# Performance work log

Measured on AMD Instinct MI355X. Metric: run time of the kernel, lower is better.

## Reference

```python
import jax, jax.numpy as jnp
import numpy as np

T, N, D, H = 128, 512, 1024, 1024
LN_EPS = 1e-5


def setup_inputs() -> dict:
    key = jax.random.key(0)
    ks = jax.random.split(key, 6)
    x = jax.random.normal(ks[0], (T * N, D), jnp.float32)
    hxs = jax.random.normal(ks[1], (N, 1, H), jnp.float32)
    # binary done-masks (float, mostly 1.0 = keep hidden state, 0.0 = episode reset)
    masks = (jax.random.uniform(ks[2], (T * N, 1)) < 0.95).astype(jnp.float32)
    s = 1.0 / np.sqrt(H)
    # PyTorch GRU packed gates, order (r, z, n): weight_ih_l0 [3H, D], weight_hh_l0 [3H, H]
    W_ih = jax.random.normal(ks[3], (3 * H, D), jnp.float32) * s
    W_hh = jax.random.normal(ks[4], (3 * H, H), jnp.float32) * s
    b_ih = jnp.zeros((3 * H,), jnp.float32)  # module inits biases to 0
    b_hh = jnp.zeros((3 * H,), jnp.float32)
    gamma = jnp.ones((H,), jnp.float32)
    beta = jnp.zeros((H,), jnp.float32)
    return dict(x=x, hxs=hxs, masks=masks, W_ih=W_ih, W_hh=W_hh,
                b_ih=b_ih, b_hh=b_hh, gamma=gamma, beta=beta)


def reference(x, hxs, masks, W_ih, W_hh, b_ih, b_hh, gamma, beta):
    TN = x.shape[0]
    Nn = hxs.shape[0]
    Tt = TN // Nn
    Hd = hxs.shape[-1]
    xs = x.reshape(Tt, Nn, -1)          # [T, N, D]
    m = masks.reshape(Tt, Nn)           # [T, N]
    # Chunk starts per source: t=0 plus every t>=1 where (masks[t] == 1).any().
    # At a chunk start the hidden state is multiplied by masks[t] (broadcast over layers);
    # a scan with a per-step conditional mask-multiply is exactly equivalent to the
    # torch loop over chunks.
    reset = jnp.concatenate([jnp.ones((1,), bool), jnp.any(m[1:] == 1.0, axis=-1)])
    # Batch the input projection across all T*N tokens (one big GEMM): [T, N, 3H]
    xp = jnp.einsum('tnd,gd->tng', xs, W_ih) + b_ih
    h0 = hxs[:, 0, :]                   # recurrent_N == 1 -> [N, H]

    def step(h, inp):
        xp_t, m_t, r_t = inp
        h = jnp.where(r_t, h * m_t[:, None], h)
        hp = h @ W_hh.T + b_hh          # [N, 3H]
        xr, xz, xn = jnp.split(xp_t, 3, axis=-1)
        hr, hz, hn = jnp.split(hp, 3, axis=-1)
        r = jax.nn.sigmoid(xr + hr)
        z = jax.nn.sigmoid(xz + hz)
        n = jnp.tanh(xn + r * hn)
        h_new = (1.0 - z) * n + z * h
        return h_new, h_new

    h_last, outs = jax.lax.scan(step, h0, (xp, m, reset))
    y = outs.reshape(Tt * Nn, Hd)
    # LayerNorm over last dim
    mu = y.mean(-1, keepdims=True)
    var = y.var(-1, keepdims=True)
    y = (y - mu) * jax.lax.rsqrt(var + LN_EPS) * gamma + beta
    return y, h_last[:, None, :]
```

## Files before the change

kernel.cpp:

```cpp
#include <hip/hip_runtime.h>

#define T_STEPS 128
#define N_B     512
#define D_IN    1024
#define H_DIM   1024
#define G_DIM   3072
#define M_ALL   (T_STEPS * N_B)
#define CHUNK   16
#define NCHUNK  8
#define BAR_STRIDE 64

typedef short          s8v  __attribute__((ext_vector_type(8)));
typedef float          f4v  __attribute__((ext_vector_type(4)));
typedef unsigned short u4v  __attribute__((ext_vector_type(4)));

__device__ __forceinline__ unsigned short f2bf(float f) {
  union { float f; unsigned u; } v; v.f = f;
  unsigned r = v.u + 0x7FFFu + ((v.u >> 16) & 1u);
  return (unsigned short)(r >> 16);
}
__device__ __forceinline__ float bf2f(unsigned short h) {
  union { unsigned u; float f; } v; v.u = ((unsigned)h) << 16;
  return v.f;
}
__device__ __forceinline__ void async16(const void* g, void* l) {
  __builtin_amdgcn_global_load_lds(
      (const __attribute__((address_space(1))) unsigned*)g,
      (__attribute__((address_space(3))) unsigned*)l, 16, 0, 0);
}
__device__ __forceinline__ void async16_coh(const void* g, void* l) {
  __builtin_amdgcn_global_load_lds(
      (const __attribute__((address_space(1))) unsigned*)g,
      (__attribute__((address_space(3))) unsigned*)l, 16, 0, 17);
}
__device__ __forceinline__ void store_bf16_coh(unsigned short* p, unsigned short v) {
  unsigned v32 = v;
  asm volatile("global_store_short %0, %1, off sc0 sc1" :: "v"(p), "v"(v32) : "memory");
}
__device__ __forceinline__ float sigmoidf_(float x) { return 1.f / (1.f + __expf(-x)); }
__device__ __forceinline__ float tanhf_(float x)    { return 1.f - 2.f / (1.f + __expf(2.f * x)); }

__global__ void cvt_bf16(const float* __restrict__ in, unsigned short* __restrict__ out, long n4) {
  long i = (long)blockIdx.x * blockDim.x + threadIdx.x;
  long stride = (long)gridDim.x * blockDim.x;
  for (; i < n4; i += stride) {
    f4v v = *(const f4v*)(in + i * 4);
    u4v o;
    #pragma unroll
    for (int e = 0; e < 4; ++e) o[e] = f2bf(v[e]);
    *(u4v*)(out + i * 4) = o;
  }
}

__global__ void reset_kernel(const float* __restrict__ masks, int* __restrict__ reset) {
  const int t = blockIdx.x;
  __shared__ int flag;
  if (threadIdx.x == 0) flag = (t == 0) ? 1 : 0;
  __syncthreads();
  if (t > 0 && masks[(size_t)t * N_B + threadIdx.x] == 1.0f) flag = 1;
  __syncthreads();
  if (threadIdx.x == 0) reset[t] = flag;
}

__global__ __launch_bounds__(256) void gemm_xp(const unsigned short* __restrict__ A,
                                               const unsigned short* __restrict__ B,
                                               const float* __restrict__ bias,
                                               unsigned short* __restrict__ C) {
  const int m0 = blockIdx.y * 128, g0 = blockIdx.x * 128;
  const int tid = threadIdx.x, wv = tid >> 6, l = tid & 63;
  const int l15 = l & 15, l4 = l >> 4;
  const int wr = wv >> 1, wc = wv & 1;
  __shared__ unsigned short As[128 * 64], Bs[128 * 64];

  f4v zero4 = {0.f, 0.f, 0.f, 0.f};
  f4v acc[4][4];
  #pragma unroll
  for (int i = 0; i < 4; ++i)
    #pragma unroll
    for (int j = 0; j < 4; ++j) acc[i][j] = zero4;

  const int srow = l >> 3;
  const int selem = ((l & 7) ^ srow) * 8;
  const int swz_rd = (l15 & 7) << 4;

  for (int kt = 0; kt < 1024; kt += 64) {
    #pragma unroll
    for (int cc = 0; cc < 4; ++cc) {
      int s = wv * 4 + cc;
      int row = s * 8 + srow;
      async16(A + (size_t)(m0 + row) * 1024 + kt + selem, &As[s * 512]);
      async16(B + (size_t)(g0 + row) * 1024 + kt + selem, &Bs[s * 512]);
    }
    __syncthreads();
    #pragma unroll
    for (int ks = 0; ks < 2; ++ks) {
      s8v a[4], b[4];
      #pragma unroll
      for (int i = 0; i < 4; ++i) {
        int ra = wr * 64 + i * 16 + l15, rb = wc * 64 + i * 16 + l15;
        int cb = (ks * 64 + l4 * 16) ^ swz_rd;
        a[i] = *(const s8v*)((const char*)As + ra * 128 + cb);
        b[i] = *(const s8v*)((const char*)Bs + rb * 128 + cb);
      }
      #pragma unroll
      for (int i = 0; i < 4; ++i)
        #pragma unroll
        for (int j = 0; j < 4; ++j)
          acc[i][j] = __builtin_amdgcn_mfma_f32_16x16x32_bf16(a[i], b[j], acc[i][j], 0, 0, 0);
    }
    __syncthreads();
  }
  #pragma unroll
  for (int j = 0; j < 4; ++j) {
    int gcol = g0 + wc * 64 + j * 16 + l15;
    float bv = bias[gcol];
    #pragma unroll
    for (int i = 0; i < 4; ++i) {
      int mrow = m0 + wr * 64 + i * 16 + l4 * 4;
      u4v o;
      #pragma unroll
      for (int r = 0; r < 4; ++r) o[r] = f2bf(acc[i][j][r] + bv);
      *(u4v*)(C + (size_t)gcol * M_ALL + mrow) = o;
    }
  }
}

__global__ __launch_bounds__(256) void rnn_chunk7(
    const unsigned short* __restrict__ Whh,
    const unsigned short* __restrict__ xpT,
    const float* __restrict__ masks,
    const int* __restrict__ reset,
    const float* __restrict__ bhh,
    const float* __restrict__ hxs,
    unsigned short* hbuf,
    float* __restrict__ y,
    float* __restrict__ hlast,
    unsigned* bar,
    int t0) {
  const int bid = blockIdx.x;
  const int jt = bid & 31, nt = bid >> 5;
  const int j0 = jt * 32, n0 = nt * 64;
  const int tid = threadIdx.x, w = tid >> 6, l = tid & 63;
  const int l15 = l & 15, l4 = l >> 4;
  const int wn = w & 1, wj = w >> 1;
  const size_t NH = (size_t)N_B * H_DIM;

  __shared__ unsigned short Hs[3][64 * 128];
  __shared__ unsigned short Ws[3][96 * 128];
  __shared__ unsigned short xpl[3][32][64];

  const int lrow4 = l >> 4;
  const int lcb = (l & 15) * 16;
  const int swz_rd = (l15 & 7) << 4;

  const int jj = j0 + wj * 16 + l15;
  const float br = bhh[jj];
  const float bz = bhh[H_DIM + jj];
  const float bn = bhh[2 * H_DIM + jj];

  float hreg[2][4];
  {
    const float* hsrc = (t0 == 0) ? hxs : (y + (size_t)(t0 - 1) * NH);
    #pragma unroll
    for (int i = 0; i < 2; ++i)
      #pragma unroll
      for (int r = 0; r < 4; ++r)
        hreg[i][r] = hsrc[(size_t)(n0 + wn * 32 + i * 16 + l4 * 4 + r) * H_DIM + jj];
  }

  f4v zero4 = {0.f, 0.f, 0.f, 0.f};
  s8v zer8 = {0, 0, 0, 0, 0, 0, 0, 0};

  for (int ls = 0; ls < CHUNK; ++ls) {
    const int t = t0 + ls;
    const unsigned short* hread = hbuf + (size_t)(t & 1) * NH;
    unsigned short* hwrite = hbuf + (size_t)((t & 1) ^ 1) * NH;
    const int rst = reset[t];

    bool zo[2];
    #pragma unroll
    for (int i = 0; i < 2; ++i) {
      float mv = masks[(size_t)t * N_B + n0 + wn * 32 + i * 16 + l15];
      zo[i] = rst && (mv == 0.0f);
    }
    float mreg[2][4];
    #pragma unroll
    for (int i = 0; i < 2; ++i)
      #pragma unroll
      for (int r = 0; r < 4; ++r)
        mreg[i][r] = masks[(size_t)t * N_B + n0 + wn * 32 + i * 16 + l4 * 4 + r];

    f4v acc[2][3];
    #pragma unroll
    for (int i = 0; i < 2; ++i)
      #pragma unroll
      for (int g3 = 0; g3 < 3; ++g3) acc[i][g3] = zero4;

    auto stage = [&](int buf, int kt) {
      #pragma unroll
      for (int q = 0; q < 4; ++q) {
        int rb = w * 16 + q * 4;
        int row = rb + lrow4;
        int cb = lcb ^ ((row & 7) << 4);
        async16_coh(hread + (size_t)(n0 + row) * H_DIM + kt * 128 + (cb >> 1),
                    &Hs[buf][rb * 128]);
      }
      #pragma unroll
      for (int q = 0; q < 6; ++q) {
        int rb = w * 24 + q * 4;
        int row = rb + lrow4;
        int gate = row >> 5, jjl = row & 31;
        int cb = lcb ^ ((row & 7) << 4);
        async16(Whh + ((size_t)gate * H_DIM + j0 + jjl) * H_DIM + kt * 128 + (cb >> 1),
                &Ws[buf][rb * 128]);
      }
    };

    stage(0, 0); stage(1, 1); stage(2, 2);

    {
      const int jl = w * 8 + (l >> 3);
      const int nelem = ((l & 7) ^ (l >> 3)) * 8;
      #pragma unroll
      for (int g3 = 0; g3 < 3; ++g3)
        async16(xpT + (size_t)(g3 * H_DIM + j0 + jl) * M_ALL + (size_t)t * N_B + n0 + nelem,
                &xpl[g3][w * 8][0]);
    }

#define KT_BODY(KT, VM, DO_STAGE)                                              \
    {                                                                          \
      asm volatile("s_waitcnt vmcnt(" #VM ")" ::: "memory");                   \
      __builtin_amdgcn_s_barrier();                                            \
      __builtin_amdgcn_sched_barrier(0);                                       \
      if (DO_STAGE) stage((KT + 2) % 3, KT + 2);                               \
      const char* hb = (const char*)&Hs[KT % 3][0];                            \
      const char* wb = (const char*)&Ws[KT % 3][0];                            \
      _Pragma("unroll")                                                        \
      for (int ks = 0; ks < 4; ++ks) {                                         \
        const int kbb = (ks * 64 + l4 * 16) ^ swz_rd;                          \
        s8v a[2], b[3];                                                        \
        _Pragma("unroll")                                                      \
        for (int i = 0; i < 2; ++i) {                                          \
          a[i] = *(const s8v*)(hb + (wn * 32 + i * 16 + l15) * 256 + kbb);     \
          if (zo[i]) a[i] = zer8;                                              \
        }                                                                      \
        _Pragma("unroll")                                                      \
        for (int g3 = 0; g3 < 3; ++g3)                                         \
          b[g3] = *(const s8v*)(wb + (g3 * 32 + wj * 16 + l15) * 256 + kbb);   \
        _Pragma("unroll")                                                      \
        for (int i = 0; i < 2; ++i)                                            \
          _Pragma("unroll")                                                    \
          for (int g3 = 0; g3 < 3; ++g3)                                       \
            acc[i][g3] = __builtin_amdgcn_mfma_f32_16x16x32_bf16(a[i], b[g3],  \
                                                                acc[i][g3], 0, 0, 0); \
      }                                                                        \
    }

    KT_BODY(0, 23, false)
    KT_BODY(1, 13, true)
    KT_BODY(2, 13, true)
    KT_BODY(3, 10, true)
    KT_BODY(4, 10, true)
    KT_BODY(5, 10, true)
    KT_BODY(6, 10, false)
    KT_BODY(7, 0,  false)
#undef KT_BODY

    #pragma unroll
    for (int i = 0; i < 2; ++i) {
      #pragma unroll
      for (int r = 0; r < 4; ++r) {
        const int n = n0 + wn * 32 + i * 16 + l4 * 4 + r;
        const int nl = wn * 32 + i * 16 + l4 * 4 + r;
        const int jl = wj * 16 + l15;
        float hprev = hreg[i][r];
        if (rst && mreg[i][r] == 0.0f) hprev = 0.0f;
        const float hr = acc[i][0][r] + br;
        const float hz = acc[i][1][r] + bz;
        const float hn = acc[i][2][r] + bn;
        const char* xb = (const char*)&xpl[0][0][0];
        const int nb = (nl * 2) ^ ((jl & 7) << 4);
        const float xr = bf2f(*(const unsigned short*)(xb + 0 * 4096 + jl * 128 + nb));
        const float xz = bf2f(*(const unsigned short*)(xb + 1 * 4096 + jl * 128 + nb));
        const float xn = bf2f(*(const unsigned short*)(xb + 2 * 4096 + jl * 128 + nb));
        const float rg = sigmoidf_(xr + hr);
        const float zg = sigmoidf_(xz + hz);
        const float ng = tanhf_(xn + rg * hn);
        const float hnew = (1.f - zg) * ng + zg * hprev;
        hreg[i][r] = hnew;
        const size_t gidx = (size_t)n * H_DIM + jj;
        y[(size_t)t * NH + gidx] = hnew;
        store_bf16_coh(hwrite + gidx, f2bf(hnew));
        if (t == T_STEPS - 1) hlast[gidx] = hnew;
      }
    }

    __syncthreads();
    if (tid == 0) {
      __hip_atomic_fetch_add(&bar[nt * BAR_STRIDE], 1u, __ATOMIC_RELAXED, __HIP_MEMORY_SCOPE_AGENT);
      const unsigned tgt = 32u * (unsigned)(ls + 1);
      while (__hip_atomic_load(&bar[nt * BAR_STRIDE], __ATOMIC_RELAXED, __HIP_MEMORY_SCOPE_AGENT) < tgt)
        __builtin_amdgcn_s_sleep(1);
    }
    __syncthreads();
  }
}

__global__ __launch_bounds__(256) void ln_kernel(float* __restrict__ y,
                                                 const float* __restrict__ gamma,
                                                 const float* __restrict__ beta) {
  const size_t row = blockIdx.x;
  float* p = y + row * (size_t)H_DIM;
  const int tid = threadIdx.x;
  f4v v = *(const f4v*)(p + tid * 4);
  float s = v[0] + v[1] + v[2] + v[3];
  float q = v[0] * v[0] + v[1] * v[1] + v[2] * v[2] + v[3] * v[3];
  #pragma unroll
  for (int off = 32; off > 0; off >>= 1) {
    s += __shfl_down(s, off);
    q += __shfl_down(q, off);
  }
  __shared__ float sb[8];
  const int wid = tid >> 6, lid = tid & 63;
  if (lid == 0) { sb[wid] = s; sb[4 + wid] = q; }
  __syncthreads();
  float S = sb[0] + sb[1] + sb[2] + sb[3];
  float Q = sb[4] + sb[5] + sb[6] + sb[7];
  float mean = S * (1.f / H_DIM);
  float var = Q * (1.f / H_DIM) - mean * mean;
  float inv = rsqrtf(var + 1e-5f);
  f4v g4 = *(const f4v*)(gamma + tid * 4);
  f4v b4 = *(const f4v*)(beta + tid * 4);
  f4v o;
  #pragma unroll
  for (int e = 0; e < 4; ++e) o[e] = (v[e] - mean) * inv * g4[e] + b4[e];
  *(f4v*)(p + tid * 4) = o;
}

extern "C" void kernel_launch(void* const* d_in, const int* in_sizes, int n_in,
                              void* d_out, int out_size, void* d_ws, size_t ws_size,
                              hipStream_t stream) {
  const float* x     = (const float*)d_in[0];
  const float* hxs   = (const float*)d_in[1];
  const float* masks = (const float*)d_in[2];
  const float* W_ih  = (const float*)d_in[3];
  const float* W_hh  = (const float*)d_in[4];
  const float* b_ih  = (const float*)d_in[5];
  const float* b_hh  = (const float*)d_in[6];
  const float* gamma = (const float*)d_in[7];
  const float* beta  = (const float*)d_in[8];
  float* y = (float*)d_out;
  float* hlast = y + (size_t)T_STEPS * N_B * H_DIM;

  char* ws = (char*)d_ws;
  unsigned short* Wih_bf = (unsigned short*)ws;  ws += (size_t)G_DIM * D_IN * 2;
  unsigned short* Whh_bf = (unsigned short*)ws;  ws += (size_t)G_DIM * H_DIM * 2;
  unsigned short* xc_bf  = (unsigned short*)ws;  ws += (size_t)M_ALL * D_IN * 2;
  unsigned short* xpT_bf = (unsigned short*)ws;  ws += (size_t)G_DIM * M_ALL * 2;
  unsigned short* hbuf   = (unsigned short*)ws;  ws += (size_t)2 * N_B * H_DIM * 2;
  unsigned* bars         = (unsigned*)ws;        ws += NCHUNK * 8 * BAR_STRIDE * sizeof(unsigned);
  int* reset             = (int*)ws;             ws += 512;

  hipMemsetAsync(bars, 0, NCHUNK * 8 * BAR_STRIDE * sizeof(unsigned), stream);
  cvt_bf16<<<1024, 256, 0, stream>>>(W_ih, Wih_bf, (long)G_DIM * D_IN / 4);
  cvt_bf16<<<1024, 256, 0, stream>>>(W_hh, Whh_bf, (long)G_DIM * H_DIM / 4);
  cvt_bf16<<<512, 256, 0, stream>>>(hxs, hbuf, (long)N_B * H_DIM / 4);
  reset_kernel<<<128, 512, 0, stream>>>(masks, reset);
  cvt_bf16<<<4096, 256, 0, stream>>>(x, xc_bf, (long)M_ALL * D_IN / 4);

  dim3 gg(G_DIM / 128, M_ALL / 128);
  gemm_xp<<<gg, 256, 0, stream>>>(xc_bf, Wih_bf, b_ih, xpT_bf);

  for (int ck = 0; ck < NCHUNK; ++ck) {
    rnn_chunk7<<<256, 256, 0, stream>>>(Whh_bf, xpT_bf, masks, reset, b_hh, hxs, hbuf,
                                        y, hlast, bars + (size_t)ck * 8 * BAR_STRIDE,
                                        ck * CHUNK);
  }

  ln_kernel<<<T_STEPS * N_B, 256, 0, stream>>>(y, gamma, beta);
}
```

Baseline: 2.287 ms.

## Fuse recurrent chunks into one persistent kernel and prefetch next step during barrier

```diff
diff --git a/kernel.cpp b/kernel.cpp
--- a/kernel.cpp
+++ b/kernel.cpp
@@ -6,8 +6,6 @@
 #define H_DIM   1024
 #define G_DIM   3072
 #define M_ALL   (T_STEPS * N_B)
-#define CHUNK   16
-#define NCHUNK  8
 #define BAR_STRIDE 64
 
 typedef short          s8v  __attribute__((ext_vector_type(8)));
@@ -125,7 +123,7 @@
   }
 }
 
-__global__ __launch_bounds__(256) void rnn_chunk7(
+__global__ __launch_bounds__(256, 1) void rnn_all(
     const unsigned short* __restrict__ Whh,
     const unsigned short* __restrict__ xpT,
     const float* __restrict__ masks,
@@ -135,8 +133,7 @@
     unsigned short* hbuf,
     float* __restrict__ y,
     float* __restrict__ hlast,
-    unsigned* bar,
-    int t0) {
+    unsigned* bar) {
   const int bid = blockIdx.x;
   const int jt = bid & 31, nt = bid >> 5;
   const int j0 = jt * 32, n0 = nt * 64;
@@ -159,80 +156,79 @@
   const float bn = bhh[2 * H_DIM + jj];
 
   float hreg[2][4];
-  {
-    const float* hsrc = (t0 == 0) ? hxs : (y + (size_t)(t0 - 1) * NH);
-    #pragma unroll
-    for (int i = 0; i < 2; ++i)
-      #pragma unroll
-      for (int r = 0; r < 4; ++r)
-        hreg[i][r] = hsrc[(size_t)(n0 + wn * 32 + i * 16 + l4 * 4 + r) * H_DIM + jj];
-  }
+  #pragma unroll
+  for (int i = 0; i < 2; ++i)
+    #pragma unroll
+    for (int r = 0; r < 4; ++r)
+      hreg[i][r] = hxs[(size_t)(n0 + wn * 32 + i * 16 + l4 * 4 + r) * H_DIM + jj];
 
   f4v zero4 = {0.f, 0.f, 0.f, 0.f};
   s8v zer8 = {0, 0, 0, 0, 0, 0, 0, 0};
 
-  for (int ls = 0; ls < CHUNK; ++ls) {
-    const int t = t0 + ls;
+  auto stageH = [&](const unsigned short* hread, int buf, int kt) {
+    #pragma unroll
+    for (int q = 0; q < 4; ++q) {
+      int rb = w * 16 + q * 4;
+      int row = rb + lrow4;
+      int cb = lcb ^ ((row & 7) << 4);
+      async16_coh(hread + (size_t)(n0 + row) * H_DIM + kt * 128 + (cb >> 1),
+                  &Hs[buf][rb * 128]);
+    }
+  };
+  auto stageW = [&](int buf, int kt) {
+    #pragma unroll
+    for (int q = 0; q < 6; ++q) {
+      int rb = w * 24 + q * 4;
+      int row = rb + lrow4;
+      int gate = row >> 5, jjl = row & 31;
+      int cb = lcb ^ ((row & 7) << 4);
+      async16(Whh + ((size_t)gate * H_DIM + j0 + jjl) * H_DIM + kt * 128 + (cb >> 1),
+              &Ws[buf][rb * 128]);
+    }
+  };
+  auto stageXP = [&](int t) {
+    const int jl = w * 8 + (l >> 3);
+    const int nelem = ((l & 7) ^ (l >> 3)) * 8;
+    #pragma unroll
+    for (int g3 = 0; g3 < 3; ++g3)
+      async16(xpT + (size_t)(g3 * H_DIM + j0 + jl) * M_ALL + (size_t)t * N_B + n0 + nelem,
+              &xpl[g3][w * 8][0]);
+  };
+
+  int rst = reset[0];
+  bool zo[2];
+  float mreg[2][4];
+  #pragma unroll
+  for (int i = 0; i < 2; ++i) {
+    float mv = masks[(size_t)0 * N_B + n0 + wn * 32 + i * 16 + l15];
+    zo[i] = rst && (mv == 0.0f);
+  }
+  #pragma unroll
+  for (int i = 0; i < 2; ++i)
+    #pragma unroll
+    for (int r = 0; r < 4; ++r)
+      mreg[i][r] = masks[(size_t)0 * N_B + n0 + wn * 32 + i * 16 + l4 * 4 + r];
+  stageW(0, 0); stageW(1, 1); stageW(2, 2);
+  stageXP(0);
+
+  for (int t = 0; t < T_STEPS; ++t) {
     const unsigned short* hread = hbuf + (size_t)(t & 1) * NH;
     unsigned short* hwrite = hbuf + (size_t)((t & 1) ^ 1) * NH;
-    const int rst = reset[t];
-
-    bool zo[2];
-    #pragma unroll
-    for (int i = 0; i < 2; ++i) {
-      float mv = masks[(size_t)t * N_B + n0 + wn * 32 + i * 16 + l15];
-      zo[i] = rst && (mv == 0.0f);
-    }
-    float mreg[2][4];
+
+    stageH(hread, 0, 0); stageH(hread, 1, 1); stageH(hread, 2, 2);
+
+    f4v acc[2][3];
     #pragma unroll
     for (int i = 0; i < 2; ++i)
       #pragma unroll
-      for (int r = 0; r < 4; ++r)
-        mreg[i][r] = masks[(size_t)t * N_B + n0 + wn * 32 + i * 16 + l4 * 4 + r];
-
-    f4v acc[2][3];
-    #pragma unroll
-    for (int i = 0; i < 2; ++i)
-      #pragma unroll
       for (int g3 = 0; g3 < 3; ++g3) acc[i][g3] = zero4;
-
-    auto stage = [&](int buf, int kt) {
-      #pragma unroll
-      for (int q = 0; q < 4; ++q) {
-        int rb = w * 16 + q * 4;
-        int row = rb + lrow4;
-        int cb = lcb ^ ((row & 7) << 4);
-        async16_coh(hread + (size_t)(n0 + row) * H_DIM + kt * 128 + (cb >> 1),
-                    &Hs[buf][rb * 128]);
-      }
-      #pragma unroll
-      for (int q = 0; q < 6; ++q) {
-        int rb = w * 24 + q * 4;
-        int row = rb + lrow4;
-        int gate = row >> 5, jjl = row & 31;
-        int cb = lcb ^ ((row & 7) << 4);
-        async16(Whh + ((size_t)gate * H_DIM + j0 + jjl) * H_DIM + kt * 128 + (cb >> 1),
-                &Ws[buf][rb * 128]);
-      }
-    };
-
-    stage(0, 0); stage(1, 1); stage(2, 2);
-
-    {
-      const int jl = w * 8 + (l >> 3);
-      const int nelem = ((l & 7) ^ (l >> 3)) * 8;
-      #pragma unroll
-      for (int g3 = 0; g3 < 3; ++g3)
-        async16(xpT + (size_t)(g3 * H_DIM + j0 + jl) * M_ALL + (size_t)t * N_B + n0 + nelem,
-                &xpl[g3][w * 8][0]);
-    }
 
 #define KT_BODY(KT, VM, DO_STAGE)                                              \
     {                                                                          \
       asm volatile("s_waitcnt vmcnt(" #VM ")" ::: "memory");                   \
       __builtin_amdgcn_s_barrier();                                            \
       __builtin_amdgcn_sched_barrier(0);                                       \
-      if (DO_STAGE) stage((KT + 2) % 3, KT + 2);                               \
+      if (DO_STAGE) { stageH(hread, (KT + 2) % 3, KT + 2); stageW((KT + 2) % 3, KT + 2); } \
       const char* hb = (const char*)&Hs[KT % 3][0];                            \
       const char* wb = (const char*)&Ws[KT % 3][0];                            \
       _Pragma("unroll")                                                        \
@@ -256,9 +252,9 @@
       }                                                                        \
     }
 
-    KT_BODY(0, 23, false)
-    KT_BODY(1, 13, true)
-    KT_BODY(2, 13, true)
+    KT_BODY(0, 8,  false)
+    KT_BODY(1, 4,  true)
+    KT_BODY(2, 10, true)
     KT_BODY(3, 10, true)
     KT_BODY(4, 10, true)
     KT_BODY(5, 10, true)
@@ -296,13 +292,42 @@
     }
 
     __syncthreads();
+
+    int rstN = 0;
+    bool zoN[2] = {false, false};
+    float mregN[2][4];
+    if (t + 1 < T_STEPS) {
+      rstN = reset[t + 1];
+      #pragma unroll
+      for (int i = 0; i < 2; ++i) {
+        float mv = masks[(size_t)(t + 1) * N_B + n0 + wn * 32 + i * 16 + l15];
+        zoN[i] = rstN && (mv == 0.0f);
+      }
+      #pragma unroll
+      for (int i = 0; i < 2; ++i)
+        #pragma unroll
+        for (int r = 0; r < 4; ++r)
+          mregN[i][r] = masks[(size_t)(t + 1) * N_B + n0 + wn * 32 + i * 16 + l4 * 4 + r];
+      stageW(0, 0); stageW(1, 1); stageW(2, 2);
+      stageXP(t + 1);
+    }
+
     if (tid == 0) {
       __hip_atomic_fetch_add(&bar[nt * BAR_STRIDE], 1u, __ATOMIC_RELAXED, __HIP_MEMORY_SCOPE_AGENT);
-      const unsigned tgt = 32u * (unsigned)(ls + 1);
+      const unsigned tgt = 32u * (unsigned)(t + 1);
       while (__hip_atomic_load(&bar[nt * BAR_STRIDE], __ATOMIC_RELAXED, __HIP_MEMORY_SCOPE_AGENT) < tgt)
         __builtin_amdgcn_s_sleep(1);
     }
-    __syncthreads();
+    __builtin_amdgcn_s_barrier();
+    __builtin_amdgcn_sched_barrier(0);
+
+    rst = rstN;
+    #pragma unroll
+    for (int i = 0; i < 2; ++i) {
+      zo[i] = zoN[i];
+      #pragma unroll
+      for (int r = 0; r < 4; ++r) mreg[i][r] = mregN[i][r];
+    }
   }
 }
 
@@ -358,10 +383,10 @@
   unsigned short* xc_bf  = (unsigned short*)ws;  ws += (size_t)M_ALL * D_IN * 2;
   unsigned short* xpT_bf = (unsigned short*)ws;  ws += (size_t)G_DIM * M_ALL * 2;
   unsigned short* hbuf   = (unsigned short*)ws;  ws += (size_t)2 * N_B * H_DIM * 2;
-  unsigned* bars         = (unsigned*)ws;        ws += NCHUNK * 8 * BAR_STRIDE * sizeof(unsigned);
+  unsigned* bars         = (unsigned*)ws;        ws += 8 * BAR_STRIDE * sizeof(unsigned);
   int* reset             = (int*)ws;             ws += 512;
 
-  hipMemsetAsync(bars, 0, NCHUNK * 8 * BAR_STRIDE * sizeof(unsigned), stream);
+  hipMemsetAsync(bars, 0, 8 * BAR_STRIDE * sizeof(unsigned), stream);
   cvt_bf16<<<1024, 256, 0, stream>>>(W_ih, Wih_bf, (long)G_DIM * D_IN / 4);
   cvt_bf16<<<1024, 256, 0, stream>>>(W_hh, Whh_bf, (long)G_DIM * H_DIM / 4);
   cvt_bf16<<<512, 256, 0, stream>>>(hxs, hbuf, (long)N_B * H_DIM / 4);
@@ -371,11 +396,8 @@
   dim3 gg(G_DIM / 128, M_ALL / 128);
   gemm_xp<<<gg, 256, 0, stream>>>(xc_bf, Wih_bf, b_ih, xpT_bf);
 
-  for (int ck = 0; ck < NCHUNK; ++ck) {
-    rnn_chunk7<<<256, 256, 0, stream>>>(Whh_bf, xpT_bf, masks, reset, b_hh, hxs, hbuf,
-                                        y, hlast, bars + (size_t)ck * 8 * BAR_STRIDE,
-                                        ck * CHUNK);
-  }
+  rnn_all<<<256, 256, 0, stream>>>(Whh_bf, xpT_bf, masks, reset, b_hh,
+                                   hxs, hbuf, y, hlast, bars);
 
   ln_kernel<<<T_STEPS * N_B, 256, 0, stream>>>(y, gamma, beta);
 }
```

Measured after the change: 2.266 ms, median of 2. Within noise of the previous version (-0.9%).
